# Kernel tuning notes

Hardware: AMD Instinct MI355X
Metric: run time of the kernel (lower is better)

The kernel has to match this reference:

```python
import jax, jax.numpy as jnp
import numpy as np


def setup_inputs() -> dict:
    key = jax.random.key(0)
    ks = jax.random.split(key, 8)
    B, L, D, N, K = 4, 4096, 1024, 64, 4
    return {
        "x": jax.random.normal(ks[0], (B, L, D), dtype=jnp.float32),
        "conv_w": jax.random.normal(ks[1], (K, 1, D), dtype=jnp.float32) * 0.1,
        "conv_b": jnp.zeros((D,), dtype=jnp.float32),
        "Wp": jax.random.normal(ks[2], (D, 2 * N), dtype=jnp.float32) * (1.0 / np.sqrt(D)),
        "bp": jnp.zeros((2 * N,), dtype=jnp.float32),
        "Ws": jax.random.normal(ks[3], (D, N), dtype=jnp.float32) * (1.0 / np.sqrt(D)),
        "bs": jnp.zeros((N,), dtype=jnp.float32),
        "A_log": jax.random.normal(ks[4], (N,), dtype=jnp.float32) * 0.02,
        "dt_log": jax.random.normal(ks[5], (N,), dtype=jnp.float32) * 0.02,
        "Wo": jax.random.normal(ks[6], (N, D), dtype=jnp.float32) * (1.0 / np.sqrt(N)),
        "bo": jnp.zeros((D,), dtype=jnp.float32),
    }


def reference(x, conv_w, conv_b, Wp, bp, Ws, bs, A_log, dt_log, Wo, bo):
    B, L, D = x.shape
    K = conv_w.shape[0]
    N = Ws.shape[1]

    # causal depthwise conv: left-pad by K-1, sum K shifted slices (K is tiny)
    x_pad = jnp.pad(x, ((0, 0), (K - 1, 0), (0, 0)))
    conv = conv_b + sum(x_pad[:, k:k + L, :] * conv_w[k, 0] for k in range(K))

    proj = conv @ Wp + bp                     # [B, L, 2N]
    B_t = jax.nn.softplus(proj[..., :N])      # [B, L, N]
    C_t = jnp.tanh(proj[..., N:])             # [B, L, N]
    u = x @ Ws + bs                           # [B, L, N]

    A = -jax.nn.softplus(A_log)               # [N]
    dt = jax.nn.softplus(dt_log)              # [N]
    decay = 1.0 + dt * A                      # [N]

    def step(state, inputs):
        u_t, b_t, c_t = inputs                # each [B, N]
        state = decay * state + dt * b_t * u_t
        return state, c_t * state

    init = jnp.zeros((B, N), dtype=x.dtype)
    xs = tuple(jnp.swapaxes(a, 0, 1) for a in (u, B_t, C_t))  # time-major
    _, ys = jax.lax.scan(step, init, xs, unroll=4)            # [L, B, N]
    y = jnp.swapaxes(ys, 0, 1)                                # [B, L, N]
    return y @ Wo + bo                                        # [B, L, D]
```

## Files before the change

### kernel.cpp

```cpp
#include <hip/hip_runtime.h>

#define B_ 4
#define L_ 4096
#define D_ 1024
#define N_ 64

typedef _Float16 f16;
typedef __attribute__((ext_vector_type(8))) _Float16 half8;
typedef __attribute__((ext_vector_type(4))) float f32x4;

__device__ __forceinline__ float softplus_f(float x) {
    return fmaxf(x, 0.0f) + log1pf(__expf(-fabsf(x)));
}

__device__ __forceinline__ float tanh_f(float x) {
    float xc = fminf(fmaxf(x, -15.0f), 15.0f);
    float e = __expf(2.0f * xc);
    return (e - 1.0f) / (e + 1.0f);
}

__global__ __launch_bounds__(256) void k_prepw(
    const float* __restrict__ Wp, const float* __restrict__ Ws,
    const float* __restrict__ Wo, f16* __restrict__ WT, f16* __restrict__ WoT)
{
    int gid = blockIdx.x * 256 + threadIdx.x;
    if (gid < 24576) {
        int r = gid >> 7, kg = gid & 127;
        const float* src; int ncol, c;
        if (r < 128) { src = Wp; ncol = 128; c = r; }
        else         { src = Ws; ncol = 64;  c = r - 128; }
        f16 h[8];
        #pragma unroll
        for (int j = 0; j < 8; j++)
            h[j] = (f16)src[(size_t)(kg * 8 + j) * ncol + c];
        *(uint4*)&WT[(size_t)r * 1024 + kg * 8] = *(uint4*)h;
    } else {
        int g2 = gid - 24576;
        int d = g2 >> 3, ng = g2 & 7;
        f16 h[8];
        #pragma unroll
        for (int j = 0; j < 8; j++)
            h[j] = (f16)Wo[(size_t)(ng * 8 + j) * D_ + d];
        *(uint4*)&WoT[(size_t)d * 64 + ng * 8] = *(uint4*)h;
    }
}

__global__ __launch_bounds__(256) void k_frontend(
    const float* __restrict__ x, const float* __restrict__ conv_w,
    const float* __restrict__ conv_b, const f16* __restrict__ WT,
    const float* __restrict__ bp, const float* __restrict__ bs,
    const float* __restrict__ dt_log,
    f16* __restrict__ zT, f16* __restrict__ cT)
{
    __shared__ __align__(16) char smem[25664];
    f16*   xh  = (f16*)smem;
    f16*   ch  = (f16*)(smem + 2880);
    float* cwS = (float*)(smem + 5184);
    float* sE  = (float*)smem;

    const int tid = threadIdx.x;
    const int w = tid >> 6, lane = tid & 63;
    const int r = lane & 15, q = lane >> 4;
    const int T0 = blockIdx.x * 16;
    const int bb = T0 >> 12;
    const int l0 = T0 & (L_ - 1);
    const int cw0 = w * 48;

    f32x4 acc[3] = {};
    float4 rA, rB;

    #pragma unroll
    for (int i = 0; i < 5; i++) {
        int idx = tid + 256 * i;
        float4 v = (idx < 1024) ? ((const float4*)conv_w)[idx]
                                : ((const float4*)conv_b)[idx - 1024];
        ((float4*)cwS)[idx] = v;
    }

    #define LDX(c0)                                                          \
        {                                                                    \
            {                                                                \
                int row = tid >> 4, g = tid & 15;                            \
                int l = l0 + row - 4;                                        \
                float4 v = make_float4(0.f, 0.f, 0.f, 0.f);                  \
                if (l >= 0)                                                  \
                    v = *(const float4*)&x[((size_t)(bb * L_ + l)) * D_      \
                                           + (c0) + g * 4];                  \
                rA = v;                                                      \
            }                                                                \
            if (tid < 64) {                                                  \
                int row = 16 + (tid >> 4), g = tid & 15;                     \
                int l = l0 + row - 4;               \
                rB = *(const float4*)&x[((size_t)(bb * L_ + l)) * D_         \
                                        + (c0) + g * 4];                     \
            }                                                                \
        }

    LDX(0);
    for (int c = 0; c < 16; c++) {
        __syncthreads();
        {
            int row = tid >> 4, g = tid & 15;
            f16 h[4] = {(f16)rA.x, (f16)rA.y, (f16)rA.z, (f16)rA.w};
            *(uint2*)&xh[row * 72 + g * 4] = *(uint2*)h;
            if (tid < 64) {
                int row2 = 16 + (tid >> 4);
                f16 h2[4] = {(f16)rB.x, (f16)rB.y, (f16)rB.z, (f16)rB.w};
                *(uint2*)&xh[row2 * 72 + g * 4] = *(uint2*)h2;
            }
        }
        __syncthreads();

        const int k0 = c * 64;

        {
            const int row = tid >> 4;
            const int d4 = (tid & 15) * 4;
            const int dg = k0 + d4;
            f32x4 w0 = *(const f32x4*)&cwS[dg];
            f32x4 w1 = *(const f32x4*)&cwS[1024 + dg];
            f32x4 w2 = *(const f32x4*)&cwS[2048 + dg];
            f32x4 w3 = *(const f32x4*)&cwS[3072 + dg];
            f32x4 cb = *(const f32x4*)&cwS[4096 + dg];
            f16 x0[4], x1[4], x2[4], x3[4], ho[4];
            *(uint2*)x0 = *(const uint2*)&xh[(row + 1) * 72 + d4];
            *(uint2*)x1 = *(const uint2*)&xh[(row + 2) * 72 + d4];
            *(uint2*)x2 = *(const uint2*)&xh[(row + 3) * 72 + d4];
            *(uint2*)x3 = *(const uint2*)&xh[(row + 4) * 72 + d4];
            #pragma unroll
            for (int j = 0; j < 4; j++) {
                float s = cb[j];
                s = fmaf(w0[j], (float)x0[j], s);
                s = fmaf(w1[j], (float)x1[j], s);
                s = fmaf(w2[j], (float)x2[j], s);
                s = fmaf(w3[j], (float)x3[j], s);
                ho[j] = (f16)s;
            }
            *(uint2*)&ch[row * 72 + d4] = *(uint2*)ho;
        }
        __syncthreads();

        half8 af[2][3];
        #pragma unroll
        for (int ks = 0; ks < 2; ks++)
            #pragma unroll
            for (int mf = 0; mf < 3; mf++)
                af[ks][mf] = *(const half8*)&WT[
                    (size_t)(cw0 + mf * 16 + r) * 1024 + k0 + ks * 32 + q * 8];

        if (c < 15) LDX((c + 1) * 64);

        const bool needC = (cw0 < 128);
        const bool needR = (cw0 + 32 >= 128);
        #pragma unroll
        for (int ks = 0; ks < 2; ks++) {
            const int kl = ks * 32 + q * 8;
            half8 bc = {}, br = {};
            if (needC) bc = *(const half8*)&ch[r * 72 + kl];
            if (needR) br = *(const half8*)&xh[(r + 4) * 72 + kl];
            #pragma unroll
            for (int mf = 0; mf < 3; mf++) {
                const bool useConv = (cw0 + mf * 16) < 128;
                acc[mf] = __builtin_amdgcn_mfma_f32_16x16x32_f16(
                    af[ks][mf], useConv ? bc : br, acc[mf], 0, 0, 0);
            }
        }
    }

    float* sB = sE;
    float* sC = sE + 16 * 68;
    float* sU = sE + 2 * 16 * 68;
    __syncthreads();
    #pragma unroll
    for (int mf = 0; mf < 3; mf++) {
        const int cb4 = cw0 + mf * 16 + q * 4;
        const int seg = cb4 >> 6;
        const int cl = cb4 & 63;
        const float4 bb4 = (seg == 2) ? *(const float4*)&bs[cl]
                                      : *(const float4*)&bp[cb4];
        float* dst = (seg == 0) ? sB : (seg == 1 ? sC : sU);
        float v0 = acc[mf][0] + bb4.x;
        float v1 = acc[mf][1] + bb4.y;
        float v2 = acc[mf][2] + bb4.z;
        float v3 = acc[mf][3] + bb4.w;
        if (seg == 0) {
            v0 = softplus_f(v0); v1 = softplus_f(v1);
            v2 = softplus_f(v2); v3 = softplus_f(v3);
        } else if (seg == 1) {
            v0 = tanh_f(v0); v1 = tanh_f(v1);
            v2 = tanh_f(v2); v3 = tanh_f(v3);
        }
        float4 vv = {v0, v1, v2, v3};
        *(float4*)&dst[r * 68 + cl] = vv;
    }
    __syncthreads();

    {
        const int n = tid >> 2, tg = tid & 3;
        const float dtv = softplus_f(dt_log[n]);
        f16 hz[4], hc[4];
        #pragma unroll
        for (int j = 0; j < 4; j++) {
            const int t = tg * 4 + j;
            hz[j] = (f16)(dtv * sB[t * 68 + n] * sU[t * 68 + n]);
            hc[j] = (f16)sC[t * 68 + n];
        }
        size_t o = ((size_t)(bb * N_ + n)) * L_ + l0 + tg * 4;
        *(uint2*)&zT[o] = *(uint2*)hz;
        *(uint2*)&cT[o] = *(uint2*)hc;
    }
    #undef LDX
}

#define ZI(i) ((i) + ((i) >> 4))
__global__ __launch_bounds__(256) void k_scan(
    const f16* __restrict__ zT, const f16* __restrict__ cT,
    const float* __restrict__ A_log, const float* __restrict__ dt_log,
    f16* __restrict__ yH)
{
    __shared__ float zs[4352];
    __shared__ float cs[4352];
    __shared__ float sA[4], sB[4];
    const int bn = blockIdx.x;
    const int n = bn & (N_ - 1);
    const int tid = threadIdx.x;
    const int lane = tid & 63, w = tid >> 6;
    const f16* zp = zT + (size_t)bn * L_;
    const f16* cp = cT + (size_t)bn * L_;

    #pragma unroll
    for (int it = 0; it < 2; it++) {
        int i = tid * 8 + it * 2048;
        uint4 rz = *(const uint4*)(zp + i);
        uint4 rc = *(const uint4*)(cp + i);
        const f16* hz = (const f16*)&rz;
        const f16* hc = (const f16*)&rc;
        #pragma unroll
        for (int k = 0; k < 8; k++) {
            zs[ZI(i + k)] = (float)hz[k];
            cs[ZI(i + k)] = (float)hc[k];
        }
    }
    __syncthreads();

    float dtv = softplus_f(dt_log[n]);
    float Av = -softplus_f(A_log[n]);
    float dec = fmaf(dtv, Av, 1.0f);

    const int base = tid * 17;
    float s = 0.0f;
    #pragma unroll
    for (int j = 0; j < 16; j++) s = fmaf(dec, s, zs[base + j]);

    float d2 = dec * dec, d4 = d2 * d2, d8 = d4 * d4, d16 = d8 * d8;

    float Ag = d16, Bg = s;
    #pragma unroll
    for (int off = 1; off < 64; off <<= 1) {
        float Ap = __shfl_up(Ag, off);
        float Bp = __shfl_up(Bg, off);
        if (lane >= off) { Bg = fmaf(Ag, Bp, Bg); Ag *= Ap; }
    }
    if (lane == 63) { sA[w] = Ag; sB[w] = Bg; }
    __syncthreads();

    float Bc = 0.0f;
    for (int i = 0; i < w; i++) Bc = fmaf(sA[i], Bc, sB[i]);
    float Ae = __shfl_up(Ag, 1);
    float Be = __shfl_up(Bg, 1);
    if (lane == 0) { Ae = 1.0f; Be = 0.0f; }
    float carry = fmaf(Ae, Bc, Be);

    float st = carry;
    #pragma unroll
    for (int j = 0; j < 16; j++) {
        st = fmaf(dec, st, zs[base + j]);
        zs[base + j] = cs[base + j] * st;
    }
    __syncthreads();

    f16* yp = yH + (size_t)bn * L_;
    #pragma unroll
    for (int it = 0; it < 2; it++) {
        int i = tid * 8 + it * 2048;
        f16 h[8];
        #pragma unroll
        for (int k = 0; k < 8; k++) h[k] = (f16)zs[ZI(i + k)];
        *(uint4*)&yp[i] = *(uint4*)h;
    }
}
#undef ZI

__global__ __launch_bounds__(256) void k_out(
    const f16* __restrict__ yH, const f16* __restrict__ WoT,
    const float* __restrict__ bo, float* __restrict__ out)
{
    __shared__ __align__(16) f16 ys[64 * 72];
    const int tid = threadIdx.x;
    const int w = tid >> 6, lane = tid & 63;
    const int r = lane & 15, q = lane >> 4;
    const int T0 = blockIdx.x * 64;
    const int bb = T0 >> 12, l0 = T0 & (L_ - 1);
    const int dw = blockIdx.y * 128 + w * 32;

    {
        const int n = tid & 63, tg = tid >> 6;
        #pragma unroll
        for (int h2 = 0; h2 < 2; h2++) {
            uint4 v = *(const uint4*)&yH[((size_t)(bb * N_ + n)) * L_ + l0 + tg * 16 + h2 * 8];
            const f16* hh = (const f16*)&v;
            #pragma unroll
            for (int j = 0; j < 8; j++)
                ys[(tg * 16 + h2 * 8 + j) * 72 + n] = hh[j];
        }
    }
    __syncthreads();

    f32x4 acc[2][4] = {};
    #pragma unroll
    for (int ks = 0; ks < 2; ks++) {
        const int kk = ks * 32 + q * 8;
        half8 af[2];
        #pragma unroll
        for (int mf = 0; mf < 2; mf++)
            af[mf] = *(const half8*)&WoT[(size_t)(dw + mf * 16 + r) * 64 + kk];
        #pragma unroll
        for (int nf = 0; nf < 4; nf++) {
            half8 bf = *(const half8*)&ys[(nf * 16 + r) * 72 + kk];
            #pragma unroll
            for (int mf = 0; mf < 2; mf++)
                acc[mf][nf] = __builtin_amdgcn_mfma_f32_16x16x32_f16(
                    af[mf], bf, acc[mf][nf], 0, 0, 0);
        }
    }

    #pragma unroll
    for (int mf = 0; mf < 2; mf++) {
        const int d = dw + mf * 16 + q * 4;
        const float4 bb4 = *(const float4*)&bo[d];
        #pragma unroll
        for (int nf = 0; nf < 4; nf++) {
            const int t = T0 + nf * 16 + r;
            float4 o = {acc[mf][nf][0] + bb4.x, acc[mf][nf][1] + bb4.y,
                        acc[mf][nf][2] + bb4.z, acc[mf][nf][3] + bb4.w};
            *(float4*)&out[(size_t)t * D_ + d] = o;
        }
    }
}

extern "C" void kernel_launch(void* const* d_in, const int* in_sizes, int n_in,
                              void* d_out, int out_size, void* d_ws, size_t ws_size,
                              hipStream_t stream) {
    const float* x      = (const float*)d_in[0];
    const float* conv_w = (const float*)d_in[1];
    const float* conv_b = (const float*)d_in[2];
    const float* Wp     = (const float*)d_in[3];
    const float* bp     = (const float*)d_in[4];
    const float* Ws     = (const float*)d_in[5];
    const float* bs     = (const float*)d_in[6];
    const float* A_log  = (const float*)d_in[7];
    const float* dt_log = (const float*)d_in[8];
    const float* Wo     = (const float*)d_in[9];
    const float* bo     = (const float*)d_in[10];
    float* out = (float*)d_out;

    char* wsp = (char*)d_ws;
    f16* WT  = (f16*)wsp;
    f16* WoT = (f16*)(wsp + 393216);
    f16* zT  = (f16*)(wsp + 524288);
    f16* cT  = (f16*)(wsp + 2621440);
    f16* yH  = (f16*)(wsp + 4718592);

    k_prepw<<<dim3(128), dim3(256), 0, stream>>>(Wp, Ws, Wo, WT, WoT);
    k_frontend<<<dim3(B_ * L_ / 16), dim3(256), 0, stream>>>(
        x, conv_w, conv_b, WT, bp, bs, dt_log, zT, cT);
    k_scan<<<dim3(B_ * N_), dim3(256), 0, stream>>>(zT, cT, A_log, dt_log, yH);
    k_out<<<dim3(B_ * L_ / 64, D_ / 128), dim3(256), 0, stream>>>(yH, WoT, bo, out);
}
```

Measured before the change: 191.2 us.

## Widen frontend K-chunks to 256 and coalesce weight-prep reads

The frontend projection kernel now walks the reduction dimension in 4 chunks of 256 instead of 16 chunks of 64. This cuts barrier count and loop overhead, and lets the conv compute 4 rows per thread with a sliding register window. Weight loads are split into two batches interleaved with the next x prefetch, and launch bounds request 4 blocks per CU. The weight-prep kernel's index mapping is changed so adjacent threads read adjacent columns (coalesced). In exchange, shared memory and register use per block go up, which may limit occupancy.

Measured after the change: 195.6 us. 1.02x slower.

```diff
diff --git a/kernel.cpp b/kernel.cpp
--- a/kernel.cpp
+++ b/kernel.cpp
@@ -17,6 +17,12 @@
     float xc = fminf(fmaxf(x, -15.0f), 15.0f);
     float e = __expf(2.0f * xc);
     return (e - 1.0f) / (e + 1.0f);
+}
+
+__device__ __forceinline__ void barrier_raw() {
+    asm volatile("" ::: "memory");
+    __builtin_amdgcn_s_barrier();
+    asm volatile("" ::: "memory");
 }
 
 __global__ __launch_bounds__(256) void k_prepw(
@@ -24,19 +30,24 @@
     const float* __restrict__ Wo, f16* __restrict__ WT, f16* __restrict__ WoT)
 {
     int gid = blockIdx.x * 256 + threadIdx.x;
-    if (gid < 24576) {
-        int r = gid >> 7, kg = gid & 127;
-        const float* src; int ncol, c;
-        if (r < 128) { src = Wp; ncol = 128; c = r; }
-        else         { src = Ws; ncol = 64;  c = r - 128; }
+    if (gid < 16384) {
+        int c = gid & 127, kg = gid >> 7;
         f16 h[8];
         #pragma unroll
         for (int j = 0; j < 8; j++)
-            h[j] = (f16)src[(size_t)(kg * 8 + j) * ncol + c];
-        *(uint4*)&WT[(size_t)r * 1024 + kg * 8] = *(uint4*)h;
+            h[j] = (f16)Wp[(size_t)(kg * 8 + j) * 128 + c];
+        *(uint4*)&WT[(size_t)c * 1024 + kg * 8] = *(uint4*)h;
+    } else if (gid < 24576) {
+        int idx = gid - 16384;
+        int c = idx & 63, kg = idx >> 6;
+        f16 h[8];
+        #pragma unroll
+        for (int j = 0; j < 8; j++)
+            h[j] = (f16)Ws[(size_t)(kg * 8 + j) * 64 + c];
+        *(uint4*)&WT[(size_t)(128 + c) * 1024 + kg * 8] = *(uint4*)h;
     } else {
-        int g2 = gid - 24576;
-        int d = g2 >> 3, ng = g2 & 7;
+        int idx = gid - 24576;
+        int d = idx & 1023, ng = idx >> 10;
         f16 h[8];
         #pragma unroll
         for (int j = 0; j < 8; j++)
@@ -45,17 +56,20 @@
     }
 }
 
-__global__ __launch_bounds__(256) void k_frontend(
+#define CHD 256
+#define NCH 4
+#define XS  264
+__global__ __launch_bounds__(256, 4) void k_frontend(
     const float* __restrict__ x, const float* __restrict__ conv_w,
     const float* __restrict__ conv_b, const f16* __restrict__ WT,
     const float* __restrict__ bp, const float* __restrict__ bs,
     const float* __restrict__ dt_log,
     f16* __restrict__ zT, f16* __restrict__ cT)
 {
-    __shared__ __align__(16) char smem[25664];
+    __shared__ __align__(16) char smem[39488];
     f16*   xh  = (f16*)smem;
-    f16*   ch  = (f16*)(smem + 2880);
-    float* cwS = (float*)(smem + 5184);
+    f16*   ch  = (f16*)(smem + 10560);
+    float* cwS = (float*)(smem + 19008);
     float* sE  = (float*)smem;
 
     const int tid = threadIdx.x;
@@ -67,7 +81,7 @@
     const int cw0 = w * 48;
 
     f32x4 acc[3] = {};
-    float4 rA, rB;
+    float4 rA[5];
 
     #pragma unroll
     for (int i = 0; i < 5; i++) {
@@ -79,91 +93,111 @@
 
     #define LDX(c0)                                                          \
         {                                                                    \
-            {                                                                \
-                int row = tid >> 4, g = tid & 15;                            \
+            _Pragma("unroll")                                                \
+            for (int s = 0; s < 5; s++) {                                    \
+                int idx = tid + 256 * s;                                     \
+                int row = idx >> 6, g = idx & 63;                            \
                 int l = l0 + row - 4;                                        \
                 float4 v = make_float4(0.f, 0.f, 0.f, 0.f);                  \
                 if (l >= 0)                                                  \
                     v = *(const float4*)&x[((size_t)(bb * L_ + l)) * D_      \
                                            + (c0) + g * 4];                  \
-                rA = v;                                                      \
+                rA[s] = v;                                                   \
             }                                                                \
-            if (tid < 64) {                                                  \
-                int row = 16 + (tid >> 4), g = tid & 15;                     \
-                int l = l0 + row - 4;               \
-                rB = *(const float4*)&x[((size_t)(bb * L_ + l)) * D_         \
-                                        + (c0) + g * 4];                     \
-            }                                                                \
         }
 
     LDX(0);
-    for (int c = 0; c < 16; c++) {
+    for (int c = 0; c < NCH; c++) {
+        barrier_raw();
+        #pragma unroll
+        for (int s = 0; s < 5; s++) {
+            int idx = tid + 256 * s;
+            int row = idx >> 6, g = idx & 63;
+            f16 h[4] = {(f16)rA[s].x, (f16)rA[s].y, (f16)rA[s].z, (f16)rA[s].w};
+            *(uint2*)&xh[row * XS + g * 4] = *(uint2*)h;
+        }
         __syncthreads();
+
+        const int k0 = c * CHD;
+
         {
-            int row = tid >> 4, g = tid & 15;
-            f16 h[4] = {(f16)rA.x, (f16)rA.y, (f16)rA.z, (f16)rA.w};
-            *(uint2*)&xh[row * 72 + g * 4] = *(uint2*)h;
-            if (tid < 64) {
-                int row2 = 16 + (tid >> 4);
-                f16 h2[4] = {(f16)rB.x, (f16)rB.y, (f16)rB.z, (f16)rB.w};
-                *(uint2*)&xh[row2 * 72 + g * 4] = *(uint2*)h2;
-            }
-        }
-        __syncthreads();
-
-        const int k0 = c * 64;
-
-        {
-            const int row = tid >> 4;
-            const int d4 = (tid & 15) * 4;
+            const int r0 = (tid >> 6) * 4;
+            const int d4 = (tid & 63) * 4;
             const int dg = k0 + d4;
             f32x4 w0 = *(const f32x4*)&cwS[dg];
             f32x4 w1 = *(const f32x4*)&cwS[1024 + dg];
             f32x4 w2 = *(const f32x4*)&cwS[2048 + dg];
             f32x4 w3 = *(const f32x4*)&cwS[3072 + dg];
             f32x4 cb = *(const f32x4*)&cwS[4096 + dg];
-            f16 x0[4], x1[4], x2[4], x3[4], ho[4];
-            *(uint2*)x0 = *(const uint2*)&xh[(row + 1) * 72 + d4];
-            *(uint2*)x1 = *(const uint2*)&xh[(row + 2) * 72 + d4];
-            *(uint2*)x2 = *(const uint2*)&xh[(row + 3) * 72 + d4];
-            *(uint2*)x3 = *(const uint2*)&xh[(row + 4) * 72 + d4];
+            uint2 win[4];
+            win[0] = *(const uint2*)&xh[(r0 + 1) * XS + d4];
+            win[1] = *(const uint2*)&xh[(r0 + 2) * XS + d4];
+            win[2] = *(const uint2*)&xh[(r0 + 3) * XS + d4];
             #pragma unroll
-            for (int j = 0; j < 4; j++) {
-                float s = cb[j];
-                s = fmaf(w0[j], (float)x0[j], s);
-                s = fmaf(w1[j], (float)x1[j], s);
-                s = fmaf(w2[j], (float)x2[j], s);
-                s = fmaf(w3[j], (float)x3[j], s);
-                ho[j] = (f16)s;
+            for (int t = 0; t < 4; t++) {
+                win[3] = *(const uint2*)&xh[(r0 + t + 4) * XS + d4];
+                const f16* x0 = (const f16*)&win[0];
+                const f16* x1 = (const f16*)&win[1];
+                const f16* x2 = (const f16*)&win[2];
+                const f16* x3 = (const f16*)&win[3];
+                f16 ho[4];
+                #pragma unroll
+                for (int j = 0; j < 4; j++) {
+                    float s = cb[j];
+                    s = fmaf(w0[j], (float)x0[j], s);
+                    s = fmaf(w1[j], (float)x1[j], s);
+                    s = fmaf(w2[j], (float)x2[j], s);
+                    s = fmaf(w3[j], (float)x3[j], s);
+                    ho[j] = (f16)s;
+                }
+                *(uint2*)&ch[(r0 + t) * XS + d4] = *(uint2*)ho;
+                win[0] = win[1]; win[1] = win[2]; win[2] = win[3];
             }
-            *(uint2*)&ch[row * 72 + d4] = *(uint2*)ho;
         }
         __syncthreads();
-
-        half8 af[2][3];
-        #pragma unroll
-        for (int ks = 0; ks < 2; ks++)
-            #pragma unroll
-            for (int mf = 0; mf < 3; mf++)
-                af[ks][mf] = *(const half8*)&WT[
-                    (size_t)(cw0 + mf * 16 + r) * 1024 + k0 + ks * 32 + q * 8];
-
-        if (c < 15) LDX((c + 1) * 64);
 
         const bool needC = (cw0 < 128);
         const bool needR = (cw0 + 32 >= 128);
-        #pragma unroll
-        for (int ks = 0; ks < 2; ks++) {
+        const bool uc0 = (cw0      < 128);
+        const bool uc1 = (cw0 + 16 < 128);
+        const bool uc2 = (cw0 + 32 < 128);
+
+        half8 afA[4][3];
+        #pragma unroll
+        for (int ks = 0; ks < 4; ks++) {
+            const int kk = k0 + ks * 32 + q * 8;
+            afA[ks][0] = *(const half8*)&WT[(size_t)(cw0 +      r) * 1024 + kk];
+            afA[ks][1] = *(const half8*)&WT[(size_t)(cw0 + 16 + r) * 1024 + kk];
+            afA[ks][2] = *(const half8*)&WT[(size_t)(cw0 + 32 + r) * 1024 + kk];
+        }
+        #pragma unroll
+        for (int ks = 0; ks < 4; ks++) {
             const int kl = ks * 32 + q * 8;
             half8 bc = {}, br = {};
-            if (needC) bc = *(const half8*)&ch[r * 72 + kl];
-            if (needR) br = *(const half8*)&xh[(r + 4) * 72 + kl];
-            #pragma unroll
-            for (int mf = 0; mf < 3; mf++) {
-                const bool useConv = (cw0 + mf * 16) < 128;
-                acc[mf] = __builtin_amdgcn_mfma_f32_16x16x32_f16(
-                    af[ks][mf], useConv ? bc : br, acc[mf], 0, 0, 0);
-            }
+            if (needC) bc = *(const half8*)&ch[r * XS + kl];
+            if (needR) br = *(const half8*)&xh[(r + 4) * XS + kl];
+            acc[0] = __builtin_amdgcn_mfma_f32_16x16x32_f16(afA[ks][0], uc0 ? bc : br, acc[0], 0, 0, 0);
+            acc[1] = __builtin_amdgcn_mfma_f32_16x16x32_f16(afA[ks][1], uc1 ? bc : br, acc[1], 0, 0, 0);
+            acc[2] = __builtin_amdgcn_mfma_f32_16x16x32_f16(afA[ks][2], uc2 ? bc : br, acc[2], 0, 0, 0);
+        }
+        half8 afB[4][3];
+        #pragma unroll
+        for (int ks = 0; ks < 4; ks++) {
+            const int kk = k0 + 128 + ks * 32 + q * 8;
+            afB[ks][0] = *(const half8*)&WT[(size_t)(cw0 +      r) * 1024 + kk];
+            afB[ks][1] = *(const half8*)&WT[(size_t)(cw0 + 16 + r) * 1024 + kk];
+            afB[ks][2] = *(const half8*)&WT[(size_t)(cw0 + 32 + r) * 1024 + kk];
+        }
+        if (c < NCH - 1) LDX((c + 1) * CHD);
+        #pragma unroll
+        for (int ks = 0; ks < 4; ks++) {
+            const int kl = 128 + ks * 32 + q * 8;
+            half8 bc = {}, br = {};
+            if (needC) bc = *(const half8*)&ch[r * XS + kl];
+            if (needR) br = *(const half8*)&xh[(r + 4) * XS + kl];
+            acc[0] = __builtin_amdgcn_mfma_f32_16x16x32_f16(afB[ks][0], uc0 ? bc : br, acc[0], 0, 0, 0);
+            acc[1] = __builtin_amdgcn_mfma_f32_16x16x32_f16(afB[ks][1], uc1 ? bc : br, acc[1], 0, 0, 0);
+            acc[2] = __builtin_amdgcn_mfma_f32_16x16x32_f16(afB[ks][2], uc2 ? bc : br, acc[2], 0, 0, 0);
         }
     }
 
@@ -211,6 +245,9 @@
     }
     #undef LDX
 }
+#undef CHD
+#undef NCH
+#undef XS
 
 #define ZI(i) ((i) + ((i) >> 4))
 __global__ __launch_bounds__(256) void k_scan(
```
